# Kernel optimization log

Measured on AMD Instinct MI355X. Metric: run time of the kernel, lower is better.

## Reference

```python
import jax, jax.numpy as jnp
import numpy as np

B, D, N = 128, 768, 256  # batch, feature dim (hard-coded 768 in module), neighbors


def setup_inputs() -> dict:
    key = jax.random.key(0)
    k1, k2, k3, k4, k5, k6, k7 = jax.random.split(key, 7)
    s = 1.0 / np.sqrt(D)  # torch Linear default init scale
    return {
        "h_v": jax.random.normal(k1, (B, D, N), dtype=jnp.float32),
        "h_w": jax.random.normal(k2, (B, D, N), dtype=jnp.float32),
        "e_vw": jax.random.normal(k3, (B, D, N), dtype=jnp.float32),
        "We": jax.random.uniform(k4, (D, D), jnp.float32, -s, s),
        "be": jax.random.uniform(k5, (D,), jnp.float32, -s, s),
        "Ww": jax.random.uniform(k6, (D, D), jnp.float32, -s, s),
        "bw": jax.random.uniform(k7, (D,), jnp.float32, -s, s),
    }


def reference(h_v, h_w, e_vw, We, be, Ww, bw):
    # m_linear: message[:, :, n] = Linear_e(e_vw[:, :, n]) + Linear_w(h_w[:, :, n])
    # Fused as two batched GEMMs over all neighbors at once. h_v is unused (as in source).
    msg = (
        jnp.einsum("od,bdn->bon", We, e_vw)
        + jnp.einsum("od,bdn->bon", Ww, h_w)
        + (be + bw)[None, :, None]
    )
    return msg  # [B, 768, N]
```

## Files before the change

kernel.cpp:

```cpp
#include <hip/hip_runtime.h>


#define DD   768
#define NCOL 256
#define KTOT 1536
#define BM   192
#define BN   256
#define BK   64
#define NIT  24

typedef __bf16 bf16;
typedef __attribute__((ext_vector_type(8))) __bf16 bf16x8;
typedef __attribute__((ext_vector_type(4))) float f32x4;
typedef __attribute__((ext_vector_type(4))) unsigned int u32x4;

__device__ __forceinline__ int swz(int row, int kb) {
  return row * 128 + (kb ^ (((row ^ (row >> 3)) & 7) << 4));
}

__global__ void prep_w(const float* __restrict__ We, const float* __restrict__ Ww,
                       unsigned short* __restrict__ Wtile) {
  int i = blockIdx.x * blockDim.x + threadIdx.x;
  int t = i & 511;
  int g = i >> 9;
  int c = g % 3;
  int h = g / 3;
  int mt = h & 3, T = h >> 2;
  int o = mt * 192 + c * 64 + (t >> 3);
  int k = T * 64 + (t & 7) * 8;
  const float* src = (k < DD) ? (We + (size_t)o * DD + k)
                              : (Ww + (size_t)o * DD + (k - DD));
  f32x4 v0 = *(const f32x4*)src;
  f32x4 v1 = *(const f32x4*)(src + 4);
  union { bf16 h8[8]; u32x4 q; } u;
  u.h8[0]=(bf16)v0[0]; u.h8[1]=(bf16)v0[1]; u.h8[2]=(bf16)v0[2]; u.h8[3]=(bf16)v0[3];
  u.h8[4]=(bf16)v1[0]; u.h8[5]=(bf16)v1[1]; u.h8[6]=(bf16)v1[2]; u.h8[7]=(bf16)v1[3];
  *(u32x4*)(Wtile + (size_t)i * 8) = u.q;
}

__global__ __launch_bounds__(512, 2)
void msg_kernel(const float* __restrict__ h_w, const float* __restrict__ e_vw,
                const unsigned short* __restrict__ Wtile,
                const float* __restrict__ be, const float* __restrict__ bw,
                float* __restrict__ out) {
  __shared__ __align__(16) unsigned char smem[2 * 57344 + 768];
  float* bias_s = (float*)(smem + 114688);

  const int tid = threadIdx.x;
  const int p = blockIdx.x;
  const int slot = p >> 3;
  const int bb = (p & 7) * 16 + (slot >> 2);
  const int mt = slot & 3;
  const int bm0 = mt * 192;

  if (tid < 192) bias_s[tid] = be[bm0 + tid] + bw[bm0 + tid];

  const unsigned short* pA = Wtile + (size_t)(mt * 3) * 4096 + (size_t)tid * 8;
  const int rA = tid >> 3, kA = (tid & 7) * 16;
  int wAo[3];
  #pragma unroll
  for (int c = 0; c < 3; ++c) wAo[c] = swz(c * 64 + rA, kA);

  const int nq = tid & 63, kk = tid >> 6;
  const size_t xofs = (size_t)bb * DD * NCOL + (size_t)(kk * 8) * NCOL + nq * 4;
  const float* pE = e_vw + xofs;
  const float* pH = h_w + xofs;
  int wBo[4];
  #pragma unroll
  for (int j = 0; j < 4; ++j) wBo[j] = swz(4 * nq + j, kk * 16);

  u32x4 aR[3];
  f32x4 bR[8];

  auto issueA = [&](int T) {
    const unsigned short* q = pA + (size_t)T * 49152;
    aR[0] = *(const u32x4*)q;
    aR[1] = *(const u32x4*)(q + 4096);
    aR[2] = *(const u32x4*)(q + 8192);
  };
  auto issueB = [&](int T) {
    const float* q = (T < 12) ? (pE + (size_t)T * BK * NCOL)
                              : (pH + (size_t)(T - 12) * BK * NCOL);
    #pragma unroll
    for (int i = 0; i < 8; ++i) bR[i] = *(const f32x4*)(q + (size_t)i * NCOL);
  };
  auto storeA = [&](int buf) {
    unsigned char* base = smem + buf * 57344;
    #pragma unroll
    for (int c = 0; c < 3; ++c) *(u32x4*)(base + wAo[c]) = aR[c];
  };
  auto storeB = [&](int buf) {
    unsigned char* base = smem + buf * 57344 + 24576;
    #pragma unroll
    for (int j = 0; j < 4; ++j) {
      union { bf16 h8[8]; u32x4 q; } u;
      #pragma unroll
      for (int i = 0; i < 8; ++i) u.h8[i] = (bf16)bR[i][j];
      *(u32x4*)(base + wBo[j]) = u.q;
    }
  };

  const int lane = tid & 63, wid = tid >> 6;
  const int wm = wid >> 2, wn = wid & 3;
  const int lr = lane & 15, qk = (lane >> 4) * 16;
  f32x4 acc[6][4] = {};

  issueA(0); issueB(0);
  storeA(0); storeB(0);
  issueA(1); issueB(1);
  asm volatile("s_waitcnt lgkmcnt(0)" ::: "memory");
  __builtin_amdgcn_s_barrier();

  for (int t = 0; t < NIT; ++t) {
    const int c = t & 1;
    const unsigned char* bA = smem + c * 57344;
    const unsigned char* bB = bA + 24576;
    bf16x8 af0[6], bfv0[4], af1[6], bfv1[4];

    #pragma unroll
    for (int m = 0; m < 6; ++m)
      af0[m] = *(const bf16x8*)(bA + swz(wm * 96 + m * 16 + lr, qk));
    #pragma unroll
    for (int n = 0; n < 4; ++n)
      bfv0[n] = *(const bf16x8*)(bB + swz(wn * 64 + n * 16 + lr, qk));
    #pragma unroll
    for (int m = 0; m < 6; ++m)
      af1[m] = *(const bf16x8*)(bA + swz(wm * 96 + m * 16 + lr, 64 + qk));
    #pragma unroll
    for (int n = 0; n < 4; ++n)
      bfv1[n] = *(const bf16x8*)(bB + swz(wn * 64 + n * 16 + lr, 64 + qk));

    #pragma unroll
    for (int m = 0; m < 6; ++m)
      #pragma unroll
      for (int n = 0; n < 4; ++n)
        acc[m][n] = __builtin_amdgcn_mfma_f32_16x16x32_bf16(af0[m], bfv0[n], acc[m][n], 0, 0, 0);

    if (t < NIT - 1) { storeA(c ^ 1); storeB(c ^ 1); }
    if (t < NIT - 2) { issueA(t + 2); issueB(t + 2); }

    #pragma unroll
    for (int m = 0; m < 6; ++m)
      #pragma unroll
      for (int n = 0; n < 4; ++n)
        acc[m][n] = __builtin_amdgcn_mfma_f32_16x16x32_bf16(af1[m], bfv1[n], acc[m][n], 0, 0, 0);

    asm volatile("s_waitcnt lgkmcnt(0)" ::: "memory");
    __builtin_amdgcn_s_barrier();
  }

  float* po = out + (size_t)bb * DD * NCOL;
  const int g4 = (lane >> 4) * 4;
  #pragma unroll
  for (int m = 0; m < 6; ++m) {
    const int r0 = wm * 96 + m * 16 + g4;
    #pragma unroll
    for (int n = 0; n < 4; ++n) {
      const int col = wn * 64 + n * 16 + lr;
      #pragma unroll
      for (int j = 0; j < 4; ++j)
        po[(size_t)(bm0 + r0 + j) * NCOL + col] = acc[m][n][j] + bias_s[r0 + j];
    }
  }
}

extern "C" void kernel_launch(void* const* d_in, const int* in_sizes, int n_in,
                              void* d_out, int out_size, void* d_ws, size_t ws_size,
                              hipStream_t stream) {
  const float* h_w  = (const float*)d_in[1];
  const float* e_vw = (const float*)d_in[2];
  const float* We   = (const float*)d_in[3];
  const float* be   = (const float*)d_in[4];
  const float* Ww   = (const float*)d_in[5];
  const float* bw   = (const float*)d_in[6];
  float* out = (float*)d_out;
  unsigned short* Wtile = (unsigned short*)d_ws;

  prep_w<<<dim3(576), 256, 0, stream>>>(We, Ww, Wtile);
  msg_kernel<<<dim3(512), 512, 0, stream>>>(h_w, e_vw, Wtile, be, bw, out);
}
```

Before: 111.7 us.

## Load weight MFMA fragments directly from global memory, bypassing LDS

The weight-prep kernel now writes weights in MFMA-fragment order, so each wave can load its A operands straight from global/L2 into registers instead of staging them through shared memory. This cuts the LDS footprint per block and removes the A-tile LDS stores and reads. The cost is that each wave redundantly fetches its A fragments from global memory, and those loads are issued only after the second MFMA batch, so their latency sits right before the next iteration with no prefetch.

```diff
diff --git a/kernel.cpp b/kernel.cpp
--- a/kernel.cpp
+++ b/kernel.cpp
@@ -19,15 +19,16 @@
 }
 
 __global__ void prep_w(const float* __restrict__ We, const float* __restrict__ Ww,
-                       unsigned short* __restrict__ Wtile) {
+                       unsigned short* __restrict__ Wfrag) {
   int i = blockIdx.x * blockDim.x + threadIdx.x;
-  int t = i & 511;
-  int g = i >> 9;
-  int c = g % 3;
-  int h = g / 3;
-  int mt = h & 3, T = h >> 2;
-  int o = mt * 192 + c * 64 + (t >> 3);
-  int k = T * 64 + (t & 7) * 8;
+  int lane = i & 63;
+  int r = i >> 6;
+  int M = r % 12;  r /= 12;
+  int s = r & 1;   r >>= 1;
+  int T = r % 24;
+  int mt = r / 24;
+  int o = mt * 192 + M * 16 + (lane & 15);
+  int k = T * 64 + s * 32 + (lane >> 4) * 8;
   const float* src = (k < DD) ? (We + (size_t)o * DD + k)
                               : (Ww + (size_t)o * DD + (k - DD));
   f32x4 v0 = *(const f32x4*)src;
@@ -35,16 +36,16 @@
   union { bf16 h8[8]; u32x4 q; } u;
   u.h8[0]=(bf16)v0[0]; u.h8[1]=(bf16)v0[1]; u.h8[2]=(bf16)v0[2]; u.h8[3]=(bf16)v0[3];
   u.h8[4]=(bf16)v1[0]; u.h8[5]=(bf16)v1[1]; u.h8[6]=(bf16)v1[2]; u.h8[7]=(bf16)v1[3];
-  *(u32x4*)(Wtile + (size_t)i * 8) = u.q;
+  *(u32x4*)(Wfrag + (size_t)i * 8) = u.q;
 }
 
 __global__ __launch_bounds__(512, 2)
 void msg_kernel(const float* __restrict__ h_w, const float* __restrict__ e_vw,
-                const unsigned short* __restrict__ Wtile,
+                const unsigned short* __restrict__ Wfrag,
                 const float* __restrict__ be, const float* __restrict__ bw,
                 float* __restrict__ out) {
-  __shared__ __align__(16) unsigned char smem[2 * 57344 + 768];
-  float* bias_s = (float*)(smem + 114688);
+  __shared__ __align__(16) unsigned char smem[2 * 32768 + 768];
+  float* bias_s = (float*)(smem + 65536);
 
   const int tid = threadIdx.x;
   const int p = blockIdx.x;
@@ -55,12 +56,6 @@
 
   if (tid < 192) bias_s[tid] = be[bm0 + tid] + bw[bm0 + tid];
 
-  const unsigned short* pA = Wtile + (size_t)(mt * 3) * 4096 + (size_t)tid * 8;
-  const int rA = tid >> 3, kA = (tid & 7) * 16;
-  int wAo[3];
-  #pragma unroll
-  for (int c = 0; c < 3; ++c) wAo[c] = swz(c * 64 + rA, kA);
-
   const int nq = tid & 63, kk = tid >> 6;
   const size_t xofs = (size_t)bb * DD * NCOL + (size_t)(kk * 8) * NCOL + nq * 4;
   const float* pE = e_vw + xofs;
@@ -69,28 +64,16 @@
   #pragma unroll
   for (int j = 0; j < 4; ++j) wBo[j] = swz(4 * nq + j, kk * 16);
 
-  u32x4 aR[3];
   f32x4 bR[8];
 
-  auto issueA = [&](int T) {
-    const unsigned short* q = pA + (size_t)T * 49152;
-    aR[0] = *(const u32x4*)q;
-    aR[1] = *(const u32x4*)(q + 4096);
-    aR[2] = *(const u32x4*)(q + 8192);
-  };
   auto issueB = [&](int T) {
     const float* q = (T < 12) ? (pE + (size_t)T * BK * NCOL)
                               : (pH + (size_t)(T - 12) * BK * NCOL);
     #pragma unroll
     for (int i = 0; i < 8; ++i) bR[i] = *(const f32x4*)(q + (size_t)i * NCOL);
   };
-  auto storeA = [&](int buf) {
-    unsigned char* base = smem + buf * 57344;
-    #pragma unroll
-    for (int c = 0; c < 3; ++c) *(u32x4*)(base + wAo[c]) = aR[c];
-  };
   auto storeB = [&](int buf) {
-    unsigned char* base = smem + buf * 57344 + 24576;
+    unsigned char* base = smem + buf * 32768;
     #pragma unroll
     for (int j = 0; j < 4; ++j) {
       union { bf16 h8[8]; u32x4 q; } u;
@@ -103,29 +86,36 @@
   const int lane = tid & 63, wid = tid >> 6;
   const int wm = wid >> 2, wn = wid & 3;
   const int lr = lane & 15, qk = (lane >> 4) * 16;
+  const int wm6 = wm * 6;
   f32x4 acc[6][4] = {};
 
-  issueA(0); issueB(0);
-  storeA(0); storeB(0);
-  issueA(1); issueB(1);
+  const unsigned short* pW = Wfrag + ((size_t)mt * 24 * 2 * 12 * 64 + (size_t)lane) * 8;
+  bf16x8 af[12];
+
+  auto loadA = [&](int T) {
+    #pragma unroll
+    for (int s = 0; s < 2; ++s)
+      #pragma unroll
+      for (int m = 0; m < 6; ++m)
+        af[s * 6 + m] =
+            *(const bf16x8*)(pW + (size_t)(((T * 2 + s) * 12 + wm6 + m) * 64) * 8);
+  };
+
+  issueB(0);
+  storeB(0);
+  issueB(1);
+  loadA(0);
   asm volatile("s_waitcnt lgkmcnt(0)" ::: "memory");
   __builtin_amdgcn_s_barrier();
 
   for (int t = 0; t < NIT; ++t) {
     const int c = t & 1;
-    const unsigned char* bA = smem + c * 57344;
-    const unsigned char* bB = bA + 24576;
-    bf16x8 af0[6], bfv0[4], af1[6], bfv1[4];
+    const unsigned char* bB = smem + c * 32768;
+    bf16x8 bfv0[4], bfv1[4];
 
-    #pragma unroll
-    for (int m = 0; m < 6; ++m)
-      af0[m] = *(const bf16x8*)(bA + swz(wm * 96 + m * 16 + lr, qk));
     #pragma unroll
     for (int n = 0; n < 4; ++n)
       bfv0[n] = *(const bf16x8*)(bB + swz(wn * 64 + n * 16 + lr, qk));
-    #pragma unroll
-    for (int m = 0; m < 6; ++m)
-      af1[m] = *(const bf16x8*)(bA + swz(wm * 96 + m * 16 + lr, 64 + qk));
     #pragma unroll
     for (int n = 0; n < 4; ++n)
       bfv1[n] = *(const bf16x8*)(bB + swz(wn * 64 + n * 16 + lr, 64 + qk));
@@ -134,16 +124,18 @@
     for (int m = 0; m < 6; ++m)
       #pragma unroll
       for (int n = 0; n < 4; ++n)
-        acc[m][n] = __builtin_amdgcn_mfma_f32_16x16x32_bf16(af0[m], bfv0[n], acc[m][n], 0, 0, 0);
+        acc[m][n] = __builtin_amdgcn_mfma_f32_16x16x32_bf16(af[m], bfv0[n], acc[m][n], 0, 0, 0);
 
-    if (t < NIT - 1) { storeA(c ^ 1); storeB(c ^ 1); }
-    if (t < NIT - 2) { issueA(t + 2); issueB(t + 2); }
+    if (t < NIT - 1) storeB(c ^ 1);
+    if (t < NIT - 2) issueB(t + 2);
 
     #pragma unroll
     for (int m = 0; m < 6; ++m)
       #pragma unroll
       for (int n = 0; n < 4; ++n)
-        acc[m][n] = __builtin_amdgcn_mfma_f32_16x16x32_bf16(af1[m], bfv1[n], acc[m][n], 0, 0, 0);
+        acc[m][n] = __builtin_amdgcn_mfma_f32_16x16x32_bf16(af[6 + m], bfv1[n], acc[m][n], 0, 0, 0);
+
+    if (t < NIT - 1) loadA(t + 1);
 
     asm volatile("s_waitcnt lgkmcnt(0)" ::: "memory");
     __builtin_amdgcn_s_barrier();
@@ -174,8 +166,8 @@
   const float* Ww   = (const float*)d_in[5];
   const float* bw   = (const float*)d_in[6];
   float* out = (float*)d_out;
-  unsigned short* Wtile = (unsigned short*)d_ws;
+  unsigned short* Wfrag = (unsigned short*)d_ws;
 
-  prep_w<<<dim3(576), 256, 0, stream>>>(We, Ww, Wtile);
-  msg_kernel<<<dim3(512), 512, 0, stream>>>(h_w, e_vw, Wtile, be, bw, out);
+  prep_w<<<dim3(576), 256, 0, stream>>>(We, Ww, Wfrag);
+  msg_kernel<<<dim3(512), 512, 0, stream>>>(h_w, e_vw, Wfrag, be, bw, out);
 }
```

After: 123.0 us. 10.2% more time.
